# Kernel tuning notes

Hardware: AMD Instinct MI355X
Metric: run time of the kernel (lower is better)

The kernel has to match this reference:

```python
import jax, jax.numpy as jnp
import numpy as np

B, N, DIM = 16, 1024, 768
H, HD = 12, 64  # num_heads, head_dim


def rotate_half(x):
    x1, x2 = jnp.split(x, 2, axis=-1)
    return jnp.concatenate((-x2, x1), axis=-1)


def setup_inputs() -> dict:
    key = jax.random.key(0)
    k1, k2, k3, k4, k5 = jax.random.split(key, 5)
    x = jax.random.normal(k1, (B, N, DIM), dtype=jnp.float32)
    # precomputed 2D-RoPE angles for the 32x32 patch grid: (N, head_dim)
    sin = jax.random.uniform(k2, (N, HD), dtype=jnp.float32, minval=-1.0, maxval=1.0)
    cos = jax.random.uniform(k3, (N, HD), dtype=jnp.float32, minval=-1.0, maxval=1.0)
    # params: qkv (no bias), proj (with bias)
    W_qkv = jax.random.normal(k4, (DIM, 3 * H * HD), dtype=jnp.float32) / np.sqrt(DIM)
    W_proj = jax.random.normal(k5, (H * HD, DIM), dtype=jnp.float32) / np.sqrt(H * HD)
    b_proj = jnp.zeros((DIM,), dtype=jnp.float32)
    return {"x": x, "sin": sin, "cos": cos, "W_qkv": W_qkv, "W_proj": W_proj, "b_proj": b_proj}


def reference(x, sin, cos, W_qkv, W_proj, b_proj):
    b, n, _ = x.shape
    qkv = (x @ W_qkv).reshape(b, n, 3, H, HD)
    q, k, v = jnp.moveaxis(qkv, 2, 0)          # each (b, n, H, HD)
    q = jnp.swapaxes(q, 1, 2)                  # (b, H, n, HD)
    k = jnp.swapaxes(k, 1, 2)
    v = jnp.swapaxes(v, 1, 2)
    # RoPE (prefix_tokens=0: apply to all tokens); sin/cos broadcast (n,HD)->(1,1,n,HD)
    s = sin[None, None]
    c = cos[None, None]
    q = q * c + rotate_half(q) * s
    k = k * c + rotate_half(k) * s
    # scaled dot-product attention (non-causal, no mask, no dropout)
    scale = 1.0 / jnp.sqrt(jnp.asarray(HD, dtype=q.dtype))
    scores = jnp.einsum('bhqd,bhkd->bhqk', q, k) * scale
    attn = jax.nn.softmax(scores, axis=-1)
    out = jnp.einsum('bhqk,bhkd->bhqd', attn, v)
    out = jnp.swapaxes(out, 1, 2).reshape(b, n, H * HD)
    return out @ W_proj + b_proj
```

## Files before the change

### kernel.cpp

```cpp
#include <hip/hip_runtime.h>


typedef __attribute__((ext_vector_type(8))) _Float16 fp16x8;
typedef __attribute__((ext_vector_type(4))) _Float16 h4;
typedef __attribute__((ext_vector_type(4))) float f32x4;

#define MFMA16(a, b, c) __builtin_amdgcn_mfma_f32_16x16x32_f16(a, b, c, 0, 0, 0)

__device__ __forceinline__ float fexp2(float x) {
    float r;
    asm volatile("v_exp_f32 %0, %1\n\ts_nop 0" : "=v"(r) : "v"(x));
    return r;
}

__device__ __forceinline__ void gload16(const _Float16* g, _Float16* s) {
    __builtin_amdgcn_global_load_lds(
        (const __attribute__((address_space(1))) unsigned int*)g,
        (__attribute__((address_space(3))) unsigned int*)s, 16, 0, 0);
}

__global__ __launch_bounds__(256) void tofp16_kernel(const float* __restrict__ in,
                                                     _Float16* __restrict__ outp, int n4) {
    int i = blockIdx.x * 256 + threadIdx.x;
    if (i >= n4) return;
    float4 v = ((const float4*)in)[i];
    h4 o;
    o[0] = (_Float16)v.x;
    o[1] = (_Float16)v.y;
    o[2] = (_Float16)v.z;
    o[3] = (_Float16)v.w;
    *(h4*)(outp + (size_t)i * 4) = o;
}

__global__ __launch_bounds__(256) void ttrans_kernel(const float* __restrict__ W,
                                                     _Float16* __restrict__ outp,
                                                     int rows, int cols) {
    __shared__ float tile[32][33];
    const int c0 = blockIdx.x * 32, r0 = blockIdx.y * 32;
    const int t = threadIdx.x;
#pragma unroll
    for (int i = 0; i < 4; ++i) {
        int idx = t + i * 256;
        int r = idx >> 5, c = idx & 31;
        tile[r][c] = W[(size_t)(r0 + r) * cols + c0 + c];
    }
    __syncthreads();
#pragma unroll
    for (int i = 0; i < 4; ++i) {
        int idx = t + i * 256;
        int rp = idx >> 5, cp = idx & 31;
        outp[(size_t)(c0 + rp) * rows + r0 + cp] = (_Float16)tile[cp][rp];
    }
}

__device__ __forceinline__ void gemm_core4(
    const _Float16* __restrict__ Ag, const _Float16* __restrict__ Bg,
    _Float16* lds, int m0, int n0, f32x4 (&acc)[8][4]) {
    constexpr int BUF = 12288;
    constexpr int OB = 8192;
    const int t = threadIdx.x, l = t & 63, w = t >> 6;
    const int wr = w >> 1, wc = w & 1;

    const int scol = ((t & 3) ^ ((t >> 3) & 3)) << 3;
    const int srow = t >> 2;

    int afo[8], bfo[4];
#pragma unroll
    for (int i = 0; i < 8; ++i) {
        int r = wr * 128 + i * 16 + (l & 15);
        afo[i] = r * 32 + (((l >> 4) ^ ((r >> 1) & 3)) << 3);
    }
#pragma unroll
    for (int j = 0; j < 4; ++j) {
        int c = wc * 64 + j * 16 + (l & 15);
        bfo[j] = c * 32 + (((l >> 4) ^ ((c >> 1) & 3)) << 3);
    }

    auto stage0 = [&](int kt, int b) {
        _Float16* base = lds + b * BUF;
        const int k0 = kt * 32;
        gload16(Ag + (size_t)(m0 + srow) * 768 + k0 + scol, base + (w * 16) * 32);
        gload16(Ag + (size_t)(m0 + 64 + srow) * 768 + k0 + scol,
                base + (64 + w * 16) * 32);
        gload16(Bg + (size_t)(n0 + srow) * 768 + k0 + scol,
                base + OB + (w * 16) * 32);
        gload16(Bg + (size_t)(n0 + 64 + srow) * 768 + k0 + scol,
                base + OB + (64 + w * 16) * 32);
    };
    auto stage1 = [&](int kt, int b) {
        _Float16* base = lds + b * BUF;
        const int k0 = kt * 32;
        gload16(Ag + (size_t)(m0 + 128 + srow) * 768 + k0 + scol,
                base + (128 + w * 16) * 32);
        gload16(Ag + (size_t)(m0 + 192 + srow) * 768 + k0 + scol,
                base + (192 + w * 16) * 32);
    };

    stage0(0, 0);
    stage1(0, 0);
    stage0(1, 1);
    stage1(1, 1);
    asm volatile("s_waitcnt vmcnt(6)" ::: "memory");
    __builtin_amdgcn_s_barrier();

    for (int kt = 0; kt < 24; ++kt) {
        const int b = kt % 3;
        const int bn = (kt + 2) % 3;
        _Float16* bb = lds + b * BUF;

        if (kt < 22) stage0(kt + 2, bn);
        fp16x8 af[8], bf[4];
#pragma unroll
        for (int j = 0; j < 4; ++j) bf[j] = *(const fp16x8*)(bb + OB + bfo[j]);
#pragma unroll
        for (int i = 0; i < 4; ++i) af[i] = *(const fp16x8*)(bb + afo[i]);
        __builtin_amdgcn_s_barrier();
        asm volatile("s_waitcnt lgkmcnt(0)" ::: "memory");
        __builtin_amdgcn_s_setprio(1);
#pragma unroll
        for (int i = 0; i < 4; ++i)
#pragma unroll
            for (int j = 0; j < 4; ++j) acc[i][j] = MFMA16(af[i], bf[j], acc[i][j]);
        __builtin_amdgcn_s_setprio(0);
        __builtin_amdgcn_s_barrier();

        if (kt < 22) stage1(kt + 2, bn);
#pragma unroll
        for (int i = 4; i < 8; ++i) af[i] = *(const fp16x8*)(bb + afo[i]);
        __builtin_amdgcn_s_barrier();
        asm volatile("s_waitcnt lgkmcnt(0)" ::: "memory");
        __builtin_amdgcn_s_setprio(1);
#pragma unroll
        for (int i = 4; i < 8; ++i)
#pragma unroll
            for (int j = 0; j < 4; ++j) acc[i][j] = MFMA16(af[i], bf[j], acc[i][j]);
        __builtin_amdgcn_s_setprio(0);

        if (kt < 22)
            asm volatile("s_waitcnt vmcnt(6)" ::: "memory");
        else
            asm volatile("s_waitcnt vmcnt(0)" ::: "memory");
        __builtin_amdgcn_s_barrier();
    }
}

__global__ __launch_bounds__(256, 2) void qkv_gemm(
    const _Float16* __restrict__ Ag, const _Float16* __restrict__ Bg,
    const float* __restrict__ sinp, const float* __restrict__ cosp,
    _Float16* __restrict__ Qf, _Float16* __restrict__ Kf,
    _Float16* __restrict__ Vt) {
    __shared__ _Float16 lds[3 * 12288];
    const int t = threadIdx.x, l = t & 63, w = t >> 6;
    const int wr = w >> 1, wc = w & 1;

    const int bid = blockIdx.x;
    const int xcd = bid & 7, local = bid >> 3;
    const int m0 = (xcd * 8 + (local & 7)) * 256;
    const int n0 = (local >> 3) * 128;

    f32x4 acc[8][4];
#pragma unroll
    for (int i = 0; i < 8; ++i)
#pragma unroll
        for (int j = 0; j < 4; ++j) acc[i][j] = (f32x4){0.f, 0.f, 0.f, 0.f};

    gemm_core4(Ag, Bg, lds, m0, n0, acc);

    const int colbase = n0 + wc * 64;
    const int sector = colbase / 768;
    const int h = (colbase % 768) >> 6;
    const float SC = 0.18033688011f;

    if (sector == 2) {
#pragma unroll
        for (int ms = 0; ms < 8; ++ms) {
            int mbase = m0 + wr * 128 + ms * 16 + (l >> 4) * 4;
            int b = mbase >> 10, nb = mbase & 1023;
            int bh = b * 12 + h;
#pragma unroll
            for (int ns = 0; ns < 4; ++ns) {
                int d = ns * 16 + (l & 15);
                h4 pk;
#pragma unroll
                for (int reg = 0; reg < 4; ++reg) pk[reg] = (_Float16)acc[ms][ns][reg];
                *(h4*)(Vt + ((size_t)bh * 64 + d) * 1024 + nb) = pk;
            }
        }
    } else if (sector == 0) {
#pragma unroll
        for (int ms = 0; ms < 8; ++ms) {
#pragma unroll
            for (int reg = 0; reg < 4; ++reg) {
                int m = m0 + wr * 128 + ms * 16 + (l >> 4) * 4 + reg;
                int b = m >> 10, n = m & 1023;
                size_t base = ((size_t)(b * 12 + h) * 1024 + n) * 64;
#pragma unroll
                for (int p = 0; p < 2; ++p) {
                    int d = p * 16 + (l & 15);
                    float c1 = cosp[n * 64 + d], s1 = sinp[n * 64 + d];
                    float c2 = cosp[n * 64 + d + 32], s2 = sinp[n * 64 + d + 32];
                    float vlo = acc[ms][p][reg], vhi = acc[ms][p + 2][reg];
                    Qf[base + d] = (_Float16)((vlo * c1 - vhi * s1) * SC);
                    Qf[base + d + 32] = (_Float16)((vhi * c2 + vlo * s2) * SC);
                }
            }
        }
    } else {
#pragma unroll
        for (int ms = 0; ms < 8; ++ms) {
#pragma unroll
            for (int reg = 0; reg < 4; ++reg) {
                int m = m0 + wr * 128 + ms * 16 + (l >> 4) * 4 + reg;
                int b = m >> 10, n = m & 1023;
                size_t base = ((size_t)(b * 12 + h) * 1024 + n) * 64;
#pragma unroll
                for (int p = 0; p < 2; ++p) {
                    int d = p * 16 + (l & 15);
                    float c1 = cosp[n * 64 + d], s1 = sinp[n * 64 + d];
                    float c2 = cosp[n * 64 + d + 32], s2 = sinp[n * 64 + d + 32];
                    float vlo = acc[ms][p][reg], vhi = acc[ms][p + 2][reg];
                    Kf[base + d] = (_Float16)(vlo * c1 - vhi * s1);
                    Kf[base + d + 32] = (_Float16)(vhi * c2 + vlo * s2);
                }
            }
        }
    }
}

__global__ __launch_bounds__(256, 2) void proj_gemm(
    const _Float16* __restrict__ Ag, const _Float16* __restrict__ Bg,
    const float* __restrict__ bias, float* __restrict__ out) {
    __shared__ _Float16 lds[3 * 12288];
    const int t = threadIdx.x, l = t & 63, w = t >> 6;
    const int wr = w >> 1, wc = w & 1;

    const int bid = blockIdx.x;
    const int xcd = bid & 7, local = bid >> 3;
    const int m0 = (xcd * 8 + (local & 7)) * 256;
    const int n0 = (local >> 3) * 128;

    f32x4 acc[8][4];
#pragma unroll
    for (int i = 0; i < 8; ++i)
#pragma unroll
        for (int j = 0; j < 4; ++j) acc[i][j] = (f32x4){0.f, 0.f, 0.f, 0.f};

    gemm_core4(Ag, Bg, lds, m0, n0, acc);

#pragma unroll
    for (int ms = 0; ms < 8; ++ms) {
#pragma unroll
        for (int ns = 0; ns < 4; ++ns) {
            int col = n0 + wc * 64 + ns * 16 + (l & 15);
            float bv = bias[col];
#pragma unroll
            for (int reg = 0; reg < 4; ++reg) {
                int m = m0 + wr * 128 + ms * 16 + ((l >> 4) << 2) + reg;
                out[(size_t)m * 768 + col] = acc[ms][ns][reg] + bv;
            }
        }
    }
}

__global__ __launch_bounds__(256, 3) void attn_kernel(
    const _Float16* __restrict__ Qf, const _Float16* __restrict__ Kfg,
    const _Float16* __restrict__ Vtg, _Float16* __restrict__ aof) {
    __shared__ _Float16 khs[2][64][64];
    __shared__ _Float16 vts[2][64][64];
    __shared__ _Float16 pbuf[4][32][72];

    const int t = threadIdx.x, l = t & 63, w = t >> 6;
    const int flat = blockIdx.x;
    const int xcd = flat & 7, idx = flat >> 3;
    const int bh = xcd * 24 + (idx >> 3);
    const int n0 = (idx & 7) * 128;
    const int bq = bh / 12, hh = bh % 12;
    const size_t base = (size_t)bh << 16;
    const int hi = l >> 4, qL = l & 15;

    fp16x8 qf[2][2];
#pragma unroll
    for (int q2 = 0; q2 < 2; ++q2)
#pragma unroll
        for (int kk = 0; kk < 2; ++kk) {
            size_t off = base + (size_t)(n0 + w * 32 + q2 * 16 + qL) * 64 +
                         kk * 32 + (hi << 3);
            qf[q2][kk] = *(const fp16x8*)(Qf + off);
        }

    const int r0 = w * 16;
    const int srow = l >> 3;
    const int scol = ((l & 7) ^ srow) << 3;
    const _Float16* kf_src = Kfg + base + (size_t)(r0 + srow) * 64 + scol;
    const _Float16* vt_src = Vtg + base + (size_t)(r0 + srow) * 1024 + scol;

    int kfo[4][2];
#pragma unroll
    for (int c = 0; c < 4; ++c)
#pragma unroll
        for (int kk = 0; kk < 2; ++kk) {
            int row = c * 16 + qL;
            int col16 = (kk << 2) | hi;
            kfo[c][kk] = row * 64 + ((col16 ^ (row & 7)) << 3);
        }

    f32x4 ot[4][2];
    float l_part[2] = {0.f, 0.f};
#pragma unroll
    for (int q2 = 0; q2 < 2; ++q2)
#pragma unroll
        for (int dt = 0; dt < 4; ++dt) ot[dt][q2] = (f32x4){0.f, 0.f, 0.f, 0.f};

    auto stage = [&](int kt, int b) {
        const _Float16* ks = kf_src + (size_t)kt * 4096;
        gload16(ks, &khs[b][r0][0]);
        gload16(ks + 512, &khs[b][r0 + 8][0]);
        const _Float16* vs = vt_src + kt * 64;
        gload16(vs, &vts[b][r0][0]);
        gload16(vs + 8 * 1024, &vts[b][r0 + 8][0]);
    };

    stage(0, 0);
    __syncthreads();

    for (int kt = 0; kt < 16; ++kt) {
        const int cur = kt & 1;
        if (kt < 15) stage(kt + 1, cur ^ 1);

        const _Float16* kb = &khs[cur][0][0];
        const _Float16* vb = &vts[cur][0][0];

        f32x4 s[4][2];
#pragma unroll
        for (int c = 0; c < 4; ++c) {
            fp16x8 kf0 = *(const fp16x8*)(kb + kfo[c][0]);
            fp16x8 kf1 = *(const fp16x8*)(kb + kfo[c][1]);
#pragma unroll
            for (int q2 = 0; q2 < 2; ++q2) {
                f32x4 a = (f32x4){0.f, 0.f, 0.f, 0.f};
                a = MFMA16(kf0, qf[q2][0], a);
                a = MFMA16(kf1, qf[q2][1], a);
                s[c][q2] = a;
            }
        }

#pragma unroll
        for (int q2 = 0; q2 < 2; ++q2) {
            const int prow = q2 * 16 + qL;
            float lsum = 0.f;
#pragma unroll
            for (int c = 0; c < 4; ++c) {
                float p0 = fexp2(s[c][q2][0] - 4.0f);
                float p1 = fexp2(s[c][q2][1] - 4.0f);
                float p2 = fexp2(s[c][q2][2] - 4.0f);
                float p3 = fexp2(s[c][q2][3] - 4.0f);
                lsum += (p0 + p1) + (p2 + p3);
                h4 pk;
                pk[0] = (_Float16)p0;
                pk[1] = (_Float16)p1;
                pk[2] = (_Float16)p2;
                pk[3] = (_Float16)p3;
                *(h4*)&pbuf[w][prow][c * 16 + (hi << 2)] = pk;
            }
            l_part[q2] += lsum;
        }

        fp16x8 pf[2][2];
#pragma unroll
        for (int q2 = 0; q2 < 2; ++q2)
#pragma unroll
            for (int ss = 0; ss < 2; ++ss)
                pf[q2][ss] = *(const fp16x8*)&pbuf[w][q2 * 16 + qL][ss * 32 + (hi << 3)];

#pragma unroll
        for (int dt = 0; dt < 4; ++dt) {
            fp16x8 v0 = *(const fp16x8*)(vb + kfo[dt][0]);
            fp16x8 v1 = *(const fp16x8*)(vb + kfo[dt][1]);
#pragma unroll
            for (int q2 = 0; q2 < 2; ++q2) {
                ot[dt][q2] = MFMA16(v0, pf[q2][0], ot[dt][q2]);
                ot[dt][q2] = MFMA16(v1, pf[q2][1], ot[dt][q2]);
            }
        }

        __syncthreads();
    }

#pragma unroll
    for (int q2 = 0; q2 < 2; ++q2) {
        float ls = l_part[q2];
        ls += __shfl_xor(ls, 16);
        ls += __shfl_xor(ls, 32);
        float inv = 1.0f / ls;
        int n = n0 + w * 32 + q2 * 16 + qL;
        size_t rowoff = ((size_t)(bq * 1024 + n)) * 768 + hh * 64 + (hi << 2);
#pragma unroll
        for (int dt = 0; dt < 4; ++dt) {
            h4 r;
#pragma unroll
            for (int reg = 0; reg < 4; ++reg) r[reg] = (_Float16)(ot[dt][q2][reg] * inv);
            *(h4*)(aof + rowoff + dt * 16) = r;
        }
    }
}

extern "C" void kernel_launch(void* const* d_in, const int* in_sizes, int n_in,
                              void* d_out, int out_size, void* d_ws, size_t ws_size,
                              hipStream_t stream) {
    const float* x = (const float*)d_in[0];
    const float* sinp = (const float*)d_in[1];
    const float* cosp = (const float*)d_in[2];
    const float* Wqkv = (const float*)d_in[3];
    const float* Wproj = (const float*)d_in[4];
    const float* bproj = (const float*)d_in[5];
    float* out = (float*)d_out;

    char* ws = (char*)d_ws;
    _Float16* xf  = (_Float16*)(ws);
    _Float16* wqt = (_Float16*)(ws + 25165824);
    _Float16* wpt = (_Float16*)(ws + 28704768);
    _Float16* Qf  = (_Float16*)(ws + 29884416);
    _Float16* Kf  = (_Float16*)(ws + 55050240);
    _Float16* Vt  = (_Float16*)(ws + 80216064);
    _Float16* aof = xf;

    tofp16_kernel<<<12288, 256, 0, stream>>>(x, xf, 3145728);
    ttrans_kernel<<<dim3(72, 24), 256, 0, stream>>>(Wqkv, wqt, 768, 2304);
    ttrans_kernel<<<dim3(24, 24), 256, 0, stream>>>(Wproj, wpt, 768, 768);
    qkv_gemm<<<1152, 256, 0, stream>>>(xf, wqt, sinp, cosp, Qf, Kf, Vt);
    attn_kernel<<<1536, 256, 0, stream>>>(Qf, Kf, Vt, aof);
    proj_gemm<<<384, 256, 0, stream>>>(aof, wpt, bproj, out);
}
```

Baseline: 194.6 us.

## Split GEMM block tiles across eight waves with 64x64 per-wave subtiles

The QKV and projection GEMMs now launch 512 threads per block instead of 256, while keeping the 256x128 block tile. Each wave owns a 64x64 accumulator subtile rather than 128x64, which halves the accumulator registers per wave. The global-to-LDS staging is redistributed across the eight waves, and the vmcnt waits are adjusted to match. The aim is more waves in flight for latency hiding and lower per-wave register pressure, at the cost of fewer MFMAs per LDS fragment load, more barrier participants, and a tighter register budget from the new launch bounds.

```diff
diff --git a/kernel.cpp b/kernel.cpp
--- a/kernel.cpp
+++ b/kernel.cpp
@@ -53,98 +53,90 @@
     }
 }
 
-__device__ __forceinline__ void gemm_core4(
+__device__ __forceinline__ void gemm_core8(
     const _Float16* __restrict__ Ag, const _Float16* __restrict__ Bg,
-    _Float16* lds, int m0, int n0, f32x4 (&acc)[8][4]) {
+    _Float16* lds, int m0, int n0, f32x4 (&acc)[4][4]) {
     constexpr int BUF = 12288;
     constexpr int OB = 8192;
     const int t = threadIdx.x, l = t & 63, w = t >> 6;
     const int wr = w >> 1, wc = w & 1;
+    const int hi = l >> 4, qL = l & 15;
 
     const int scol = ((t & 3) ^ ((t >> 3) & 3)) << 3;
     const int srow = t >> 2;
 
-    int afo[8], bfo[4];
-#pragma unroll
-    for (int i = 0; i < 8; ++i) {
-        int r = wr * 128 + i * 16 + (l & 15);
-        afo[i] = r * 32 + (((l >> 4) ^ ((r >> 1) & 3)) << 3);
-    }
-#pragma unroll
-    for (int j = 0; j < 4; ++j) {
-        int c = wc * 64 + j * 16 + (l & 15);
-        bfo[j] = c * 32 + (((l >> 4) ^ ((c >> 1) & 3)) << 3);
-    }
-
-    auto stage0 = [&](int kt, int b) {
+    int afo[4], bfo[4];
+#pragma unroll
+    for (int i = 0; i < 4; ++i) {
+        int r = wr * 64 + i * 16 + qL;
+        afo[i] = r * 32 + ((hi ^ ((r >> 1) & 3)) << 3);
+        int c = wc * 64 + i * 16 + qL;
+        bfo[i] = OB + c * 32 + ((hi ^ ((c >> 1) & 3)) << 3);
+    }
+
+    auto stageA = [&](int kt, int b) {
         _Float16* base = lds + b * BUF;
         const int k0 = kt * 32;
-        gload16(Ag + (size_t)(m0 + srow) * 768 + k0 + scol, base + (w * 16) * 32);
-        gload16(Ag + (size_t)(m0 + 64 + srow) * 768 + k0 + scol,
-                base + (64 + w * 16) * 32);
+        gload16(Ag + (size_t)(m0 + srow) * 768 + k0 + scol,
+                base + (w * 16) * 32);
+        gload16(Ag + (size_t)(m0 + 128 + srow) * 768 + k0 + scol,
+                base + (128 + w * 16) * 32);
+    };
+    auto stageB = [&](int kt, int b) {
+        _Float16* base = lds + b * BUF;
+        const int k0 = kt * 32;
         gload16(Bg + (size_t)(n0 + srow) * 768 + k0 + scol,
                 base + OB + (w * 16) * 32);
-        gload16(Bg + (size_t)(n0 + 64 + srow) * 768 + k0 + scol,
-                base + OB + (64 + w * 16) * 32);
     };
-    auto stage1 = [&](int kt, int b) {
-        _Float16* base = lds + b * BUF;
-        const int k0 = kt * 32;
-        gload16(Ag + (size_t)(m0 + 128 + srow) * 768 + k0 + scol,
-                base + (128 + w * 16) * 32);
-        gload16(Ag + (size_t)(m0 + 192 + srow) * 768 + k0 + scol,
-                base + (192 + w * 16) * 32);
-    };
-
-    stage0(0, 0);
-    stage1(0, 0);
-    stage0(1, 1);
-    stage1(1, 1);
-    asm volatile("s_waitcnt vmcnt(6)" ::: "memory");
+
+    stageA(0, 0);
+    stageB(0, 0);
+    stageA(1, 1);
+    stageB(1, 1);
+    asm volatile("s_waitcnt vmcnt(3)" ::: "memory");
     __builtin_amdgcn_s_barrier();
 
     for (int kt = 0; kt < 24; ++kt) {
-        const int b = kt % 3;
         const int bn = (kt + 2) % 3;
-        _Float16* bb = lds + b * BUF;
-
-        if (kt < 22) stage0(kt + 2, bn);
-        fp16x8 af[8], bf[4];
-#pragma unroll
-        for (int j = 0; j < 4; ++j) bf[j] = *(const fp16x8*)(bb + OB + bfo[j]);
-#pragma unroll
-        for (int i = 0; i < 4; ++i) af[i] = *(const fp16x8*)(bb + afo[i]);
+        _Float16* bb = lds + (kt % 3) * BUF;
+
+        if (kt < 22) stageA(kt + 2, bn);
+        fp16x8 af[4], bf[4];
+#pragma unroll
+        for (int j = 0; j < 4; ++j) bf[j] = *(const fp16x8*)(bb + bfo[j]);
+#pragma unroll
+        for (int i = 0; i < 2; ++i) af[i] = *(const fp16x8*)(bb + afo[i]);
         __builtin_amdgcn_s_barrier();
         asm volatile("s_waitcnt lgkmcnt(0)" ::: "memory");
         __builtin_amdgcn_s_setprio(1);
 #pragma unroll
-        for (int i = 0; i < 4; ++i)
+        for (int i = 0; i < 2; ++i)
 #pragma unroll
             for (int j = 0; j < 4; ++j) acc[i][j] = MFMA16(af[i], bf[j], acc[i][j]);
         __builtin_amdgcn_s_setprio(0);
         __builtin_amdgcn_s_barrier();
 
-        if (kt < 22) stage1(kt + 2, bn);
-#pragma unroll
-        for (int i = 4; i < 8; ++i) af[i] = *(const fp16x8*)(bb + afo[i]);
+        if (kt < 22) stageB(kt + 2, bn);
+#pragma unroll
+        for (int i = 2; i < 4; ++i) af[i] = *(const fp16x8*)(bb + afo[i]);
         __builtin_amdgcn_s_barrier();
         asm volatile("s_waitcnt lgkmcnt(0)" ::: "memory");
         __builtin_amdgcn_s_setprio(1);
 #pragma unroll
-        for (int i = 4; i < 8; ++i)
+        for (int i = 2; i < 4; ++i)
 #pragma unroll
             for (int j = 0; j < 4; ++j) acc[i][j] = MFMA16(af[i], bf[j], acc[i][j]);
         __builtin_amdgcn_s_setprio(0);
 
         if (kt < 22)
-            asm volatile("s_waitcnt vmcnt(6)" ::: "memory");
+            asm volatile("s_waitcnt vmcnt(3)" ::: "memory");
         else
             asm volatile("s_waitcnt vmcnt(0)" ::: "memory");
         __builtin_amdgcn_s_barrier();
     }
 }
 
-__global__ __launch_bounds__(256, 2) void qkv_gemm(
+__global__ __launch_bounds__(512, 4) void qkv_gemm(
     const _Float16* __restrict__ Ag, const _Float16* __restrict__ Bg,
     const float* __restrict__ sinp, const float* __restrict__ cosp,
     _Float16* __restrict__ Qf, _Float16* __restrict__ Kf,
@@ -152,19 +144,20 @@
     __shared__ _Float16 lds[3 * 12288];
     const int t = threadIdx.x, l = t & 63, w = t >> 6;
     const int wr = w >> 1, wc = w & 1;
+    const int hi = l >> 4, qL = l & 15;
 
     const int bid = blockIdx.x;
     const int xcd = bid & 7, local = bid >> 3;
     const int m0 = (xcd * 8 + (local & 7)) * 256;
     const int n0 = (local >> 3) * 128;
 
-    f32x4 acc[8][4];
-#pragma unroll
-    for (int i = 0; i < 8; ++i)
+    f32x4 acc[4][4];
+#pragma unroll
+    for (int i = 0; i < 4; ++i)
 #pragma unroll
         for (int j = 0; j < 4; ++j) acc[i][j] = (f32x4){0.f, 0.f, 0.f, 0.f};
 
-    gemm_core4(Ag, Bg, lds, m0, n0, acc);
+    gemm_core8(Ag, Bg, lds, m0, n0, acc);
 
     const int colbase = n0 + wc * 64;
     const int sector = colbase / 768;
@@ -173,13 +166,13 @@
 
     if (sector == 2) {
 #pragma unroll
-        for (int ms = 0; ms < 8; ++ms) {
-            int mbase = m0 + wr * 128 + ms * 16 + (l >> 4) * 4;
+        for (int ms = 0; ms < 4; ++ms) {
+            int mbase = m0 + wr * 64 + ms * 16 + hi * 4;
             int b = mbase >> 10, nb = mbase & 1023;
             int bh = b * 12 + h;
 #pragma unroll
             for (int ns = 0; ns < 4; ++ns) {
-                int d = ns * 16 + (l & 15);
+                int d = ns * 16 + qL;
                 h4 pk;
 #pragma unroll
                 for (int reg = 0; reg < 4; ++reg) pk[reg] = (_Float16)acc[ms][ns][reg];
@@ -188,15 +181,15 @@
         }
     } else if (sector == 0) {
 #pragma unroll
-        for (int ms = 0; ms < 8; ++ms) {
+        for (int ms = 0; ms < 4; ++ms) {
 #pragma unroll
             for (int reg = 0; reg < 4; ++reg) {
-                int m = m0 + wr * 128 + ms * 16 + (l >> 4) * 4 + reg;
+                int m = m0 + wr * 64 + ms * 16 + hi * 4 + reg;
                 int b = m >> 10, n = m & 1023;
                 size_t base = ((size_t)(b * 12 + h) * 1024 + n) * 64;
 #pragma unroll
                 for (int p = 0; p < 2; ++p) {
-                    int d = p * 16 + (l & 15);
+                    int d = p * 16 + qL;
                     float c1 = cosp[n * 64 + d], s1 = sinp[n * 64 + d];
                     float c2 = cosp[n * 64 + d + 32], s2 = sinp[n * 64 + d + 32];
                     float vlo = acc[ms][p][reg], vhi = acc[ms][p + 2][reg];
@@ -207,15 +200,15 @@
         }
     } else {
 #pragma unroll
-        for (int ms = 0; ms < 8; ++ms) {
+        for (int ms = 0; ms < 4; ++ms) {
 #pragma unroll
             for (int reg = 0; reg < 4; ++reg) {
-                int m = m0 + wr * 128 + ms * 16 + (l >> 4) * 4 + reg;
+                int m = m0 + wr * 64 + ms * 16 + hi * 4 + reg;
                 int b = m >> 10, n = m & 1023;
                 size_t base = ((size_t)(b * 12 + h) * 1024 + n) * 64;
 #pragma unroll
                 for (int p = 0; p < 2; ++p) {
-                    int d = p * 16 + (l & 15);
+                    int d = p * 16 + qL;
                     float c1 = cosp[n * 64 + d], s1 = sinp[n * 64 + d];
                     float c2 = cosp[n * 64 + d + 32], s2 = sinp[n * 64 + d + 32];
                     float vlo = acc[ms][p][reg], vhi = acc[ms][p + 2][reg];
@@ -227,35 +220,36 @@
     }
 }
 
-__global__ __launch_bounds__(256, 2) void proj_gemm(
+__global__ __launch_bounds__(512, 4) void proj_gemm(
     const _Float16* __restrict__ Ag, const _Float16* __restrict__ Bg,
     const float* __restrict__ bias, float* __restrict__ out) {
     __shared__ _Float16 lds[3 * 12288];
     const int t = threadIdx.x, l = t & 63, w = t >> 6;
     const int wr = w >> 1, wc = w & 1;
+    const int hi = l >> 4, qL = l & 15;
 
     const int bid = blockIdx.x;
     const int xcd = bid & 7, local = bid >> 3;
     const int m0 = (xcd * 8 + (local & 7)) * 256;
     const int n0 = (local >> 3) * 128;
 
-    f32x4 acc[8][4];
-#pragma unroll
-    for (int i = 0; i < 8; ++i)
+    f32x4 acc[4][4];
+#pragma unroll
+    for (int i = 0; i < 4; ++i)
 #pragma unroll
         for (int j = 0; j < 4; ++j) acc[i][j] = (f32x4){0.f, 0.f, 0.f, 0.f};
 
-    gemm_core4(Ag, Bg, lds, m0, n0, acc);
-
-#pragma unroll
-    for (int ms = 0; ms < 8; ++ms) {
+    gemm_core8(Ag, Bg, lds, m0, n0, acc);
+
+#pragma unroll
+    for (int ms = 0; ms < 4; ++ms) {
 #pragma unroll
         for (int ns = 0; ns < 4; ++ns) {
-            int col = n0 + wc * 64 + ns * 16 + (l & 15);
+            int col = n0 + wc * 64 + ns * 16 + qL;
             float bv = bias[col];
 #pragma unroll
             for (int reg = 0; reg < 4; ++reg) {
-                int m = m0 + wr * 128 + ms * 16 + ((l >> 4) << 2) + reg;
+                int m = m0 + wr * 64 + ms * 16 + hi * 4 + reg;
                 out[(size_t)m * 768 + col] = acc[ms][ns][reg] + bv;
             }
         }
@@ -427,7 +421,7 @@
     tofp16_kernel<<<12288, 256, 0, stream>>>(x, xf, 3145728);
     ttrans_kernel<<<dim3(72, 24), 256, 0, stream>>>(Wqkv, wqt, 768, 2304);
     ttrans_kernel<<<dim3(24, 24), 256, 0, stream>>>(Wproj, wpt, 768, 768);
-    qkv_gemm<<<1152, 256, 0, stream>>>(xf, wqt, sinp, cosp, Qf, Kf, Vt);
+    qkv_gemm<<<1152, 512, 0, stream>>>(xf, wqt, sinp, cosp, Qf, Kf, Vt);
     attn_kernel<<<1536, 256, 0, stream>>>(Qf, Kf, Vt, aof);
-    proj_gemm<<<384, 256, 0, stream>>>(aof, wpt, bproj, out);
-}
+    proj_gemm<<<384, 512, 0, stream>>>(aof, wpt, bproj, out);
+}
```

After: 194.7 us. Within noise of the previous version (+0.0%).
